# Kernel tuning notes

Hardware: AMD Instinct MI355X
Metric: run time of the kernel (lower is better)

The kernel has to match this reference:

```python
import jax, jax.numpy as jnp
import numpy as np

HIDDEN = 4544
N_HEADS = 71
HEAD_DIM = 64
ROPE_BASE = 10000.0


def _rope_cos_sin(pos, dtype):
    # Falcon rotary embedding for a single decode position `pos`.
    inv_freq = 1.0 / (ROPE_BASE ** (jnp.arange(0, HEAD_DIM, 2, dtype=jnp.float32) / HEAD_DIM))
    freqs = pos * inv_freq                      # [HEAD_DIM/2]
    emb = jnp.concatenate([freqs, freqs])       # [HEAD_DIM]
    return jnp.cos(emb).astype(dtype), jnp.sin(emb).astype(dtype)


def _rotate_half(x):
    x1, x2 = jnp.split(x, 2, axis=-1)
    return jnp.concatenate([-x2, x1], axis=-1)


def setup_inputs() -> dict:
    key = jax.random.key(0)
    ks = jax.random.split(key, 6)
    B = 32
    return {
        "hidden_states": jax.random.normal(ks[0], (1, 1, B, HIDDEN), jnp.float32) * 0.02,
        "attention_mask": jnp.zeros((B, 1, 1, 2048), jnp.float32),
        "w_qkv": jax.random.normal(ks[1], (HIDDEN, (N_HEADS + 2) * HEAD_DIM), jnp.float32) * 0.02,
        "w_dense": jax.random.normal(ks[2], (HIDDEN, HIDDEN), jnp.float32) * 0.02,
        "k_cache": jax.random.normal(ks[3], (B, 1, 2048, HEAD_DIM), jnp.float32),
        "v_cache": jax.random.normal(ks[4], (B, 1, 2048, HEAD_DIM), jnp.float32),
        "layer_past_len": 2047,
    }


def reference(hidden_states, attention_mask, w_qkv, w_dense, k_cache, v_cache, layer_past_len):
    B = hidden_states.shape[2]
    kv_len = layer_past_len + 1
    scalar = 1.0 / np.sqrt(HEAD_DIM)

    x = hidden_states.reshape(B, HIDDEN)                    # decode: [1,1,B,H] -> [B,H]
    qkv = x @ w_qkv                                          # [B, (nh+2)*hd]
    q = qkv[:, : N_HEADS * HEAD_DIM].reshape(B, N_HEADS, HEAD_DIM)
    k = qkv[:, N_HEADS * HEAD_DIM : (N_HEADS + 1) * HEAD_DIM]  # [B, hd] (single MQA KV head)
    v = qkv[:, (N_HEADS + 1) * HEAD_DIM :]                     # [B, hd]

    cos, sin = _rope_cos_sin(jnp.float32(layer_past_len), qkv.dtype)
    q = q * cos + _rotate_half(q) * sin                      # [B, nh, hd]
    k = k * cos + _rotate_half(k) * sin                      # [B, hd]

    # KV-cache scatter update at position layer_past_len
    k_cache = k_cache.at[:, 0, layer_past_len, :].set(k)
    v_cache = v_cache.at[:, 0, layer_past_len, :].set(v)

    keys = k_cache[:, 0, :kv_len, :]                         # [B, L, hd]
    vals = v_cache[:, 0, :kv_len, :]                         # [B, L, hd]

    scores = jnp.einsum("bnh,blh->bnl", q, keys) * scalar    # [B, nh, L]
    scores = scores + attention_mask[:, 0, :, :kv_len]       # mask [B,1,L] broadcast over heads
    probs = jax.nn.softmax(scores, axis=-1)
    ctx = jnp.einsum("bnl,blh->bnh", probs, vals)            # [B, nh, hd]

    out = ctx.reshape(B, HIDDEN) @ w_dense                   # [B, H]
    return out.reshape(1, 1, B, HIDDEN)
```

## Files before the change

### kernel.cpp

```cpp
#include <hip/hip_runtime.h>
#include <math.h>

#define BB    32
#define HID   4544
#define NQKV  4672
#define NKT   71
#define KVCAP 2048

__global__ __launch_bounds__(256) void gemm32v4(
    const float* __restrict__ x, const float* __restrict__ W,
    float* __restrict__ part, int N, int KSG)
{
  __shared__ float xT[64 * 32];
  int lane = threadIdx.x & 63;
  int w    = threadIdx.x >> 6;
  int r0   = w * 8;
  int c0   = blockIdx.x * 256 + lane * 4;
  bool act = c0 < N;
  int cb   = act ? c0 : 0;
  int slice = blockIdx.y;

  float acc[8][4];
#pragma unroll
  for (int r = 0; r < 8; ++r)
#pragma unroll
    for (int j = 0; j < 4; ++j) acc[r][j] = 0.f;

  for (int t = slice; t < NKT; t += KSG) {
    int k0 = t * 64;
    __syncthreads();
    {
      int r  = threadIdx.x & 31;
      int kg = threadIdx.x >> 5;
      const float* xp = x + (size_t)r * HID + k0 + kg * 8;
      float4 a = *(const float4*)xp;
      float4 b = *(const float4*)(xp + 4);
      int kk = kg * 8;
      xT[(kk + 0) * 32 + r] = a.x;
      xT[(kk + 1) * 32 + r] = a.y;
      xT[(kk + 2) * 32 + r] = a.z;
      xT[(kk + 3) * 32 + r] = a.w;
      xT[(kk + 4) * 32 + r] = b.x;
      xT[(kk + 5) * 32 + r] = b.y;
      xT[(kk + 6) * 32 + r] = b.z;
      xT[(kk + 7) * 32 + r] = b.w;
    }
    __syncthreads();

    const float* wp = W + (size_t)k0 * N + cb;

#define FMA_STEP(KK, WV)                                                  \
    {                                                                     \
      float4 xa = *(const float4*)&xT[(KK) * 32 + r0];                    \
      float4 xb = *(const float4*)&xT[(KK) * 32 + r0 + 4];                \
      acc[0][0] = fmaf(xa.x, WV.x, acc[0][0]);                            \
      acc[0][1] = fmaf(xa.x, WV.y, acc[0][1]);                            \
      acc[0][2] = fmaf(xa.x, WV.z, acc[0][2]);                            \
      acc[0][3] = fmaf(xa.x, WV.w, acc[0][3]);                            \
      acc[1][0] = fmaf(xa.y, WV.x, acc[1][0]);                            \
      acc[1][1] = fmaf(xa.y, WV.y, acc[1][1]);                            \
      acc[1][2] = fmaf(xa.y, WV.z, acc[1][2]);                            \
      acc[1][3] = fmaf(xa.y, WV.w, acc[1][3]);                            \
      acc[2][0] = fmaf(xa.z, WV.x, acc[2][0]);                            \
      acc[2][1] = fmaf(xa.z, WV.y, acc[2][1]);                            \
      acc[2][2] = fmaf(xa.z, WV.z, acc[2][2]);                            \
      acc[2][3] = fmaf(xa.z, WV.w, acc[2][3]);                            \
      acc[3][0] = fmaf(xa.w, WV.x, acc[3][0]);                            \
      acc[3][1] = fmaf(xa.w, WV.y, acc[3][1]);                            \
      acc[3][2] = fmaf(xa.w, WV.z, acc[3][2]);                            \
      acc[3][3] = fmaf(xa.w, WV.w, acc[3][3]);                            \
      acc[4][0] = fmaf(xb.x, WV.x, acc[4][0]);                            \
      acc[4][1] = fmaf(xb.x, WV.y, acc[4][1]);                            \
      acc[4][2] = fmaf(xb.x, WV.z, acc[4][2]);                            \
      acc[4][3] = fmaf(xb.x, WV.w, acc[4][3]);                            \
      acc[5][0] = fmaf(xb.y, WV.x, acc[5][0]);                            \
      acc[5][1] = fmaf(xb.y, WV.y, acc[5][1]);                            \
      acc[5][2] = fmaf(xb.y, WV.z, acc[5][2]);                            \
      acc[5][3] = fmaf(xb.y, WV.w, acc[5][3]);                            \
      acc[6][0] = fmaf(xb.z, WV.x, acc[6][0]);                            \
      acc[6][1] = fmaf(xb.z, WV.y, acc[6][1]);                            \
      acc[6][2] = fmaf(xb.z, WV.z, acc[6][2]);                            \
      acc[6][3] = fmaf(xb.z, WV.w, acc[6][3]);                            \
      acc[7][0] = fmaf(xb.w, WV.x, acc[7][0]);                            \
      acc[7][1] = fmaf(xb.w, WV.y, acc[7][1]);                            \
      acc[7][2] = fmaf(xb.w, WV.z, acc[7][2]);                            \
      acc[7][3] = fmaf(xb.w, WV.w, acc[7][3]);                            \
    }

#define LOADW(P, KB)                                                      \
    {                                                                     \
      P##0 = *(const float4*)(wp + (size_t)((KB) + 0) * N);               \
      P##1 = *(const float4*)(wp + (size_t)((KB) + 1) * N);               \
      P##2 = *(const float4*)(wp + (size_t)((KB) + 2) * N);               \
      P##3 = *(const float4*)(wp + (size_t)((KB) + 3) * N);               \
    }
#define FMA4(P, KB)                                                       \
    { FMA_STEP((KB) + 0, P##0) FMA_STEP((KB) + 1, P##1)                   \
      FMA_STEP((KB) + 2, P##2) FMA_STEP((KB) + 3, P##3) }

    float4 A0, A1, A2, A3, B0, B1, B2, B3;
    float4 C0, C1, C2, C3, D0, D1, D2, D3;
    LOADW(A, 0) LOADW(B, 4) LOADW(C, 8) LOADW(D, 12)
    FMA4(A, 0)   LOADW(A, 16)
    FMA4(B, 4)   LOADW(B, 20)
    FMA4(C, 8)   LOADW(C, 24)
    FMA4(D, 12)  LOADW(D, 28)
    FMA4(A, 16)  LOADW(A, 32)
    FMA4(B, 20)  LOADW(B, 36)
    FMA4(C, 24)  LOADW(C, 40)
    FMA4(D, 28)  LOADW(D, 44)
    FMA4(A, 32)  LOADW(A, 48)
    FMA4(B, 36)  LOADW(B, 52)
    FMA4(C, 40)  LOADW(C, 56)
    FMA4(D, 44)  LOADW(D, 60)
    FMA4(A, 48)
    FMA4(B, 52)
    FMA4(C, 56)
    FMA4(D, 60)
#undef FMA_STEP
#undef LOADW
#undef FMA4
  }

  if (act) {
#pragma unroll
    for (int r = 0; r < 8; ++r) {
      float4 v = make_float4(acc[r][0], acc[r][1], acc[r][2], acc[r][3]);
      *(float4*)&part[((size_t)slice * 32 + r0 + r) * N + c0] = v;
    }
  }
}

__global__ __launch_bounds__(256) void qkv_fix(
    const float* __restrict__ part, float* __restrict__ qkvr,
    const int* __restrict__ plen, int KSG)
{
  int u = blockIdx.x * 256 + threadIdx.x;
  int r = u / 2368, t = u % 2368;
  int past = *plen;
  const size_t SS = (size_t)32 * NQKV;

  if (t < 2304) {
    int head = t >> 5, j = t & 31;
    int c0 = head * 64 + j;
    int c1 = c0 + 32;
    const float* p = part + (size_t)r * NQKV;
    float av[8], bv[8];
#pragma unroll
    for (int i = 0; i < 8; ++i) { av[i] = 0.f; bv[i] = 0.f; }
    int s = 0;
    for (; s + 8 <= KSG; s += 8)
#pragma unroll
      for (int i = 0; i < 8; ++i) {
        const float* q = p + (size_t)(s + i) * SS;
        av[i] += q[c0]; bv[i] += q[c1];
      }
    for (; s < KSG; ++s) { av[0] += p[(size_t)s * SS + c0]; bv[0] += p[(size_t)s * SS + c1]; }
    float a = ((av[0]+av[1])+(av[2]+av[3])) + ((av[4]+av[5])+(av[6]+av[7]));
    float b = ((bv[0]+bv[1])+(bv[2]+bv[3])) + ((bv[4]+bv[5])+(bv[6]+bv[7]));
    float invf = (float)pow(10000.0, -(double)j / 32.0);
    float fr   = (float)past * invf;
    float cs = (float)cos((double)fr);
    float sn = (float)sin((double)fr);
    float o0 = a * cs - b * sn;
    float o1 = b * cs + a * sn;
    if (head < 71) { o0 *= 0.125f; o1 *= 0.125f; }
    qkvr[(size_t)r * NQKV + c0] = o0;
    qkvr[(size_t)r * NQKV + c1] = o1;
  } else {
    int c = 4608 + (t - 2304);
    const float* p = part + (size_t)r * NQKV + c;
    float av[8];
#pragma unroll
    for (int i = 0; i < 8; ++i) av[i] = 0.f;
    int s = 0;
    for (; s + 8 <= KSG; s += 8)
#pragma unroll
      for (int i = 0; i < 8; ++i) av[i] += p[(size_t)(s + i) * SS];
    for (; s < KSG; ++s) av[0] += p[(size_t)s * SS];
    qkvr[(size_t)r * NQKV + c] =
        ((av[0]+av[1])+(av[2]+av[3])) + ((av[4]+av[5])+(av[6]+av[7]));
  }
}

__global__ __launch_bounds__(256) void attn_part_k(
    const float* __restrict__ qkvr, const float* __restrict__ kc,
    const float* __restrict__ vc,   const float* __restrict__ mask,
    float* __restrict__ part,       const int* __restrict__ plen)
{
  int b     = blockIdx.x;
  int chunk = blockIdx.y;
  int w     = threadIdx.x >> 6;
  int lane  = threadIdx.x & 63;
  int h0    = w * 18;
  int past  = *plen;
  int kvlen = past + 1;
  int pos0  = chunk * 128;

  __shared__ float qsh[4608];
  __shared__ float pls[4][2][64];

  for (int i = threadIdx.x; i < 1152; i += 256) {
    float4 v = (i < 1136) ? ((const float4*)(qkvr + (size_t)b * NQKV))[i]
                          : make_float4(0.f, 0.f, 0.f, 0.f);
    ((float4*)qsh)[i] = v;
  }
  __syncthreads();

  float lh[18], oh[18];
#pragma unroll
  for (int i = 0; i < 18; ++i) { lh[i] = 0.f; oh[i] = 0.f; }

  for (int sub = 0; sub < 2; ++sub) {
    int sp0 = pos0 + sub * 64;
    if (sp0 >= kvlen) break;
    int pos = sp0 + lane;
    bool valid = pos < kvlen;
    const float* krow = (pos == past)
        ? (qkvr + (size_t)b * NQKV + 4544)
        : (kc + ((size_t)b * KVCAP + pos) * 64);
    float4 ka[16];
#pragma unroll
    for (int j = 0; j < 16; ++j) ka[j] = *(const float4*)(krow + j * 4);

    float vv[64];
#pragma unroll
    for (int p = 0; p < 64; ++p) {
      int pp = sp0 + p;
      const float* vrow = (pp == past)
          ? (qkvr + (size_t)b * NQKV + 4608)
          : (vc + ((size_t)b * KVCAP + pp) * 64);
      vv[p] = vrow[lane];
    }
    float mk = valid ? mask[(size_t)b * KVCAP + pos] : 0.f;

#pragma unroll
    for (int i = 0; i < 18; ++i) {
      int h = h0 + i;
      float s0 = 0.f, s1 = 0.f, s2 = 0.f, s3 = 0.f;
#pragma unroll
      for (int j = 0; j < 16; ++j) {
        float4 qv = *(const float4*)&qsh[h * 64 + j * 4];
        s0 = fmaf(ka[j].x, qv.x, s0);
        s1 = fmaf(ka[j].y, qv.y, s1);
        s2 = fmaf(ka[j].z, qv.z, s2);
        s3 = fmaf(ka[j].w, qv.w, s3);
      }
      float s = (s0 + s1) + (s2 + s3) + mk;
      if (!valid) s = -__builtin_inff();
      float p = __expf(s);

      pls[w][i & 1][lane] = p;
      float o0 = 0.f, o1 = 0.f, o2 = 0.f, o3 = 0.f;
      float la = 0.f, lb = 0.f;
#pragma unroll
      for (int j = 0; j < 16; ++j) {
        float4 pr = *(const float4*)&pls[w][i & 1][j * 4];
        o0 = fmaf(pr.x, vv[j * 4 + 0], o0);
        o1 = fmaf(pr.y, vv[j * 4 + 1], o1);
        o2 = fmaf(pr.z, vv[j * 4 + 2], o2);
        o3 = fmaf(pr.w, vv[j * 4 + 3], o3);
        la += pr.x + pr.y;
        lb += pr.z + pr.w;
      }
      oh[i] += (o0 + o1) + (o2 + o3);
      lh[i] += la + lb;
    }
  }

#pragma unroll
  for (int i = 0; i < 18; ++i) {
    int h = h0 + i;
    if (h >= 71) break;
    size_t base = (((size_t)b * 71 + h) * 16 + chunk) * 65;
    if (lane == 0) part[base] = lh[i];
    part[base + 1 + lane] = oh[i];
  }
}

__global__ __launch_bounds__(256) void attn_comb(
    const float* __restrict__ part, float* __restrict__ ctx)
{
  int u = blockIdx.x * 4 + (threadIdx.x >> 6);
  int lane = threadIdx.x & 63;
  if (u >= BB * 71) return;
  float L0 = 0.f, L1 = 0.f, O0 = 0.f, O1 = 0.f;
#pragma unroll
  for (int c = 0; c < 16; c += 2) {
    size_t b0 = ((size_t)u * 16 + c) * 65;
    size_t b1 = ((size_t)u * 16 + c + 1) * 65;
    L0 += part[b0]; O0 += part[b0 + 1 + lane];
    L1 += part[b1]; O1 += part[b1 + 1 + lane];
  }
  int bb = u / 71, h = u % 71;
  ctx[(size_t)bb * HID + h * 64 + lane] = (O0 + O1) / (L0 + L1);
}

__global__ __launch_bounds__(256) void sum_reduce(
    const float* __restrict__ part, float* __restrict__ out, int KSG)
{
  int u4 = blockIdx.x * 256 + threadIdx.x;
  const size_t SS4 = (size_t)32 * HID / 4;
  const float4* p = (const float4*)part + u4;
  float4 a[8];
#pragma unroll
  for (int i = 0; i < 8; ++i) a[i] = make_float4(0.f, 0.f, 0.f, 0.f);
  int s = 0;
  for (; s + 8 <= KSG; s += 8)
#pragma unroll
    for (int i = 0; i < 8; ++i) {
      float4 v = p[(size_t)(s + i) * SS4];
      a[i].x += v.x; a[i].y += v.y; a[i].z += v.z; a[i].w += v.w;
    }
  for (; s < KSG; ++s) {
    float4 v = p[(size_t)s * SS4];
    a[0].x += v.x; a[0].y += v.y; a[0].z += v.z; a[0].w += v.w;
  }
#pragma unroll
  for (int i = 1; i < 8; ++i) {
    a[0].x += a[i].x; a[0].y += a[i].y; a[0].z += a[i].z; a[0].w += a[i].w;
  }
  ((float4*)out)[u4] = a[0];
}

extern "C" void kernel_launch(void* const* d_in, const int* in_sizes, int n_in,
                              void* d_out, int out_size, void* d_ws, size_t ws_size,
                              hipStream_t stream)
{
  const float* x    = (const float*)d_in[0];
  const float* mask = (const float*)d_in[1];
  const float* wqkv = (const float*)d_in[2];
  const float* wd   = (const float*)d_in[3];
  const float* kc   = (const float*)d_in[4];
  const float* vc   = (const float*)d_in[5];
  const int*   pl   = (const int*)d_in[6];
  float* out = (float*)d_out;
  float* ws  = (float*)d_ws;

  size_t wf = ws_size / 4;
  long avail = (long)wf - 294912;
  long slots = avail / 149504;
  int KSG = (int)(slots < 1 ? 1 : (slots > NKT ? NKT : slots));

  size_t partReg = (size_t)KSG * 149504;
  if (partReg < 4795392) partReg = 4795392;
  float* part = ws;
  float* qkvr = ws + partReg;
  float* ctx  = qkvr + 149504;

  gemm32v4   <<<dim3(19, KSG), 256, 0, stream>>>(x, wqkv, part, NQKV, KSG);
  qkv_fix    <<<296,           256, 0, stream>>>(part, qkvr, pl, KSG);
  attn_part_k<<<dim3(32, 16),  256, 0, stream>>>(qkvr, kc, vc, mask, part, pl);
  attn_comb  <<<568,           256, 0, stream>>>(part, ctx);
  gemm32v4   <<<dim3(18, KSG), 256, 0, stream>>>(ctx, wd, part, HID, KSG);
  sum_reduce <<<142,           256, 0, stream>>>(part, out, KSG);
}
```

Measured before the change: 381.4 us.

## Restructure GEMM tiles to 32 rows per thread, split attention into finer chunks

The GEMM kernel now uses 128-thread blocks where each thread computes all 32 batch rows for 4 columns. Each weight float4 is loaded once per block instead of by every wave, and the loop is a rolling two-row prefetch. Attention doubles the KV chunk count to 32 (64 positions per block) so the grid has more blocks. The combine stage reads 32 partials, and the final reduction uses float2 with twice the blocks. The risks are high register pressure from 128 accumulators and more partial traffic in attention.

```diff
diff --git a/kernel.cpp b/kernel.cpp
--- a/kernel.cpp
+++ b/kernel.cpp
@@ -7,126 +7,84 @@
 #define NKT   71
 #define KVCAP 2048
 
-__global__ __launch_bounds__(256) void gemm32v4(
+__global__ __launch_bounds__(128, 2) void gemm32v5(
     const float* __restrict__ x, const float* __restrict__ W,
     float* __restrict__ part, int N, int KSG)
 {
   __shared__ float xT[64 * 32];
-  int lane = threadIdx.x & 63;
-  int w    = threadIdx.x >> 6;
-  int r0   = w * 8;
-  int c0   = blockIdx.x * 256 + lane * 4;
+  int tid = threadIdx.x;
+  int c0  = blockIdx.x * 512 + tid * 4;
   bool act = c0 < N;
-  int cb   = act ? c0 : 0;
+  int cb  = act ? c0 : 0;
   int slice = blockIdx.y;
 
-  float acc[8][4];
-#pragma unroll
-  for (int r = 0; r < 8; ++r)
+  float acc[32][4];
+#pragma unroll
+  for (int r = 0; r < 32; ++r)
 #pragma unroll
     for (int j = 0; j < 4; ++j) acc[r][j] = 0.f;
+
+  auto ROW = [&](int K, float4 pv) {
+#pragma unroll
+    for (int rg = 0; rg < 8; ++rg) {
+      float4 xv = *(const float4*)&xT[K * 32 + rg * 4];
+#pragma unroll
+      for (int q = 0; q < 4; ++q) {
+        float xs = (q == 0) ? xv.x : (q == 1) ? xv.y : (q == 2) ? xv.z : xv.w;
+        int r = rg * 4 + q;
+        acc[r][0] = fmaf(xs, pv.x, acc[r][0]);
+        acc[r][1] = fmaf(xs, pv.y, acc[r][1]);
+        acc[r][2] = fmaf(xs, pv.z, acc[r][2]);
+        acc[r][3] = fmaf(xs, pv.w, acc[r][3]);
+      }
+    }
+  };
 
   for (int t = slice; t < NKT; t += KSG) {
     int k0 = t * 64;
     __syncthreads();
     {
-      int r  = threadIdx.x & 31;
-      int kg = threadIdx.x >> 5;
-      const float* xp = x + (size_t)r * HID + k0 + kg * 8;
-      float4 a = *(const float4*)xp;
-      float4 b = *(const float4*)(xp + 4);
-      int kk = kg * 8;
-      xT[(kk + 0) * 32 + r] = a.x;
-      xT[(kk + 1) * 32 + r] = a.y;
-      xT[(kk + 2) * 32 + r] = a.z;
-      xT[(kk + 3) * 32 + r] = a.w;
-      xT[(kk + 4) * 32 + r] = b.x;
-      xT[(kk + 5) * 32 + r] = b.y;
-      xT[(kk + 6) * 32 + r] = b.z;
-      xT[(kk + 7) * 32 + r] = b.w;
+      int r  = tid & 31;
+      int kg = tid >> 5;
+      const float* xp = x + (size_t)r * HID + k0 + kg * 16;
+#pragma unroll
+      for (int q = 0; q < 4; ++q) {
+        float4 a = *(const float4*)(xp + q * 4);
+        int kk = kg * 16 + q * 4;
+        xT[(kk + 0) * 32 + r] = a.x;
+        xT[(kk + 1) * 32 + r] = a.y;
+        xT[(kk + 2) * 32 + r] = a.z;
+        xT[(kk + 3) * 32 + r] = a.w;
+      }
     }
     __syncthreads();
 
     const float* wp = W + (size_t)k0 * N + cb;
-
-#define FMA_STEP(KK, WV)                                                  \
-    {                                                                     \
-      float4 xa = *(const float4*)&xT[(KK) * 32 + r0];                    \
-      float4 xb = *(const float4*)&xT[(KK) * 32 + r0 + 4];                \
-      acc[0][0] = fmaf(xa.x, WV.x, acc[0][0]);                            \
-      acc[0][1] = fmaf(xa.x, WV.y, acc[0][1]);                            \
-      acc[0][2] = fmaf(xa.x, WV.z, acc[0][2]);                            \
-      acc[0][3] = fmaf(xa.x, WV.w, acc[0][3]);                            \
-      acc[1][0] = fmaf(xa.y, WV.x, acc[1][0]);                            \
-      acc[1][1] = fmaf(xa.y, WV.y, acc[1][1]);                            \
-      acc[1][2] = fmaf(xa.y, WV.z, acc[1][2]);                            \
-      acc[1][3] = fmaf(xa.y, WV.w, acc[1][3]);                            \
-      acc[2][0] = fmaf(xa.z, WV.x, acc[2][0]);                            \
-      acc[2][1] = fmaf(xa.z, WV.y, acc[2][1]);                            \
-      acc[2][2] = fmaf(xa.z, WV.z, acc[2][2]);                            \
-      acc[2][3] = fmaf(xa.z, WV.w, acc[2][3]);                            \
-      acc[3][0] = fmaf(xa.w, WV.x, acc[3][0]);                            \
-      acc[3][1] = fmaf(xa.w, WV.y, acc[3][1]);                            \
-      acc[3][2] = fmaf(xa.w, WV.z, acc[3][2]);                            \
-      acc[3][3] = fmaf(xa.w, WV.w, acc[3][3]);                            \
-      acc[4][0] = fmaf(xb.x, WV.x, acc[4][0]);                            \
-      acc[4][1] = fmaf(xb.x, WV.y, acc[4][1]);                            \
-      acc[4][2] = fmaf(xb.x, WV.z, acc[4][2]);                            \
-      acc[4][3] = fmaf(xb.x, WV.w, acc[4][3]);                            \
-      acc[5][0] = fmaf(xb.y, WV.x, acc[5][0]);                            \
-      acc[5][1] = fmaf(xb.y, WV.y, acc[5][1]);                            \
-      acc[5][2] = fmaf(xb.y, WV.z, acc[5][2]);                            \
-      acc[5][3] = fmaf(xb.y, WV.w, acc[5][3]);                            \
-      acc[6][0] = fmaf(xb.z, WV.x, acc[6][0]);                            \
-      acc[6][1] = fmaf(xb.z, WV.y, acc[6][1]);                            \
-      acc[6][2] = fmaf(xb.z, WV.z, acc[6][2]);                            \
-      acc[6][3] = fmaf(xb.z, WV.w, acc[6][3]);                            \
-      acc[7][0] = fmaf(xb.w, WV.x, acc[7][0]);                            \
-      acc[7][1] = fmaf(xb.w, WV.y, acc[7][1]);                            \
-      acc[7][2] = fmaf(xb.w, WV.z, acc[7][2]);                            \
-      acc[7][3] = fmaf(xb.w, WV.w, acc[7][3]);                            \
-    }
-
-#define LOADW(P, KB)                                                      \
-    {                                                                     \
-      P##0 = *(const float4*)(wp + (size_t)((KB) + 0) * N);               \
-      P##1 = *(const float4*)(wp + (size_t)((KB) + 1) * N);               \
-      P##2 = *(const float4*)(wp + (size_t)((KB) + 2) * N);               \
-      P##3 = *(const float4*)(wp + (size_t)((KB) + 3) * N);               \
-    }
-#define FMA4(P, KB)                                                       \
-    { FMA_STEP((KB) + 0, P##0) FMA_STEP((KB) + 1, P##1)                   \
-      FMA_STEP((KB) + 2, P##2) FMA_STEP((KB) + 3, P##3) }
-
-    float4 A0, A1, A2, A3, B0, B1, B2, B3;
-    float4 C0, C1, C2, C3, D0, D1, D2, D3;
-    LOADW(A, 0) LOADW(B, 4) LOADW(C, 8) LOADW(D, 12)
-    FMA4(A, 0)   LOADW(A, 16)
-    FMA4(B, 4)   LOADW(B, 20)
-    FMA4(C, 8)   LOADW(C, 24)
-    FMA4(D, 12)  LOADW(D, 28)
-    FMA4(A, 16)  LOADW(A, 32)
-    FMA4(B, 20)  LOADW(B, 36)
-    FMA4(C, 24)  LOADW(C, 40)
-    FMA4(D, 28)  LOADW(D, 44)
-    FMA4(A, 32)  LOADW(A, 48)
-    FMA4(B, 36)  LOADW(B, 52)
-    FMA4(C, 40)  LOADW(C, 56)
-    FMA4(D, 44)  LOADW(D, 60)
-    FMA4(A, 48)
-    FMA4(B, 52)
-    FMA4(C, 56)
-    FMA4(D, 60)
-#undef FMA_STEP
-#undef LOADW
-#undef FMA4
+    float4 p0 = *(const float4*)(wp + 0 * (size_t)N);
+    float4 p1 = *(const float4*)(wp + 1 * (size_t)N);
+    float4 p2 = *(const float4*)(wp + 2 * (size_t)N);
+    float4 p3 = *(const float4*)(wp + 3 * (size_t)N);
+
+#pragma unroll 1
+    for (int k = 0; k < 60; k += 2) {
+      float4 n0 = *(const float4*)(wp + (size_t)(k + 4) * N);
+      float4 n1 = *(const float4*)(wp + (size_t)(k + 5) * N);
+      ROW(k + 0, p0);
+      ROW(k + 1, p1);
+      p0 = p2; p1 = p3; p2 = n0; p3 = n1;
+    }
+    ROW(60, p0);
+    ROW(61, p1);
+    ROW(62, p2);
+    ROW(63, p3);
   }
 
   if (act) {
-#pragma unroll
-    for (int r = 0; r < 8; ++r) {
+    float* pp = part + (size_t)slice * 32 * N + c0;
+#pragma unroll
+    for (int r = 0; r < 32; ++r) {
       float4 v = make_float4(acc[r][0], acc[r][1], acc[r][2], acc[r][3]);
-      *(float4*)&part[((size_t)slice * 32 + r0 + r) * N + c0] = v;
+      *(float4*)(pp + (size_t)r * N) = v;
     }
   }
 }
@@ -195,7 +153,7 @@
   int h0    = w * 18;
   int past  = *plen;
   int kvlen = past + 1;
-  int pos0  = chunk * 128;
+  int pos0  = chunk * 64;
 
   __shared__ float qsh[4608];
   __shared__ float pls[4][2][64];
@@ -207,74 +165,71 @@
   }
   __syncthreads();
 
-  float lh[18], oh[18];
-#pragma unroll
-  for (int i = 0; i < 18; ++i) { lh[i] = 0.f; oh[i] = 0.f; }
-
-  for (int sub = 0; sub < 2; ++sub) {
-    int sp0 = pos0 + sub * 64;
-    if (sp0 >= kvlen) break;
-    int pos = sp0 + lane;
-    bool valid = pos < kvlen;
-    const float* krow = (pos == past)
-        ? (qkvr + (size_t)b * NQKV + 4544)
-        : (kc + ((size_t)b * KVCAP + pos) * 64);
-    float4 ka[16];
-#pragma unroll
-    for (int j = 0; j < 16; ++j) ka[j] = *(const float4*)(krow + j * 4);
-
-    float vv[64];
-#pragma unroll
-    for (int p = 0; p < 64; ++p) {
-      int pp = sp0 + p;
-      const float* vrow = (pp == past)
-          ? (qkvr + (size_t)b * NQKV + 4608)
-          : (vc + ((size_t)b * KVCAP + pp) * 64);
-      vv[p] = vrow[lane];
-    }
-    float mk = valid ? mask[(size_t)b * KVCAP + pos] : 0.f;
-
-#pragma unroll
+  if (pos0 >= kvlen) {
     for (int i = 0; i < 18; ++i) {
       int h = h0 + i;
-      float s0 = 0.f, s1 = 0.f, s2 = 0.f, s3 = 0.f;
-#pragma unroll
-      for (int j = 0; j < 16; ++j) {
-        float4 qv = *(const float4*)&qsh[h * 64 + j * 4];
-        s0 = fmaf(ka[j].x, qv.x, s0);
-        s1 = fmaf(ka[j].y, qv.y, s1);
-        s2 = fmaf(ka[j].z, qv.z, s2);
-        s3 = fmaf(ka[j].w, qv.w, s3);
-      }
-      float s = (s0 + s1) + (s2 + s3) + mk;
-      if (!valid) s = -__builtin_inff();
-      float p = __expf(s);
-
-      pls[w][i & 1][lane] = p;
-      float o0 = 0.f, o1 = 0.f, o2 = 0.f, o3 = 0.f;
-      float la = 0.f, lb = 0.f;
-#pragma unroll
-      for (int j = 0; j < 16; ++j) {
-        float4 pr = *(const float4*)&pls[w][i & 1][j * 4];
-        o0 = fmaf(pr.x, vv[j * 4 + 0], o0);
-        o1 = fmaf(pr.y, vv[j * 4 + 1], o1);
-        o2 = fmaf(pr.z, vv[j * 4 + 2], o2);
-        o3 = fmaf(pr.w, vv[j * 4 + 3], o3);
-        la += pr.x + pr.y;
-        lb += pr.z + pr.w;
-      }
-      oh[i] += (o0 + o1) + (o2 + o3);
-      lh[i] += la + lb;
-    }
-  }
-
-#pragma unroll
+      if (h >= 71) break;
+      size_t base = (((size_t)b * 71 + h) * 32 + chunk) * 65;
+      if (lane == 0) part[base] = 0.f;
+      part[base + 1 + lane] = 0.f;
+    }
+    return;
+  }
+
+  int pos = pos0 + lane;
+  bool valid = pos < kvlen;
+  const float* krow = (pos == past)
+      ? (qkvr + (size_t)b * NQKV + 4544)
+      : (kc + ((size_t)b * KVCAP + pos) * 64);
+  float4 ka[16];
+#pragma unroll
+  for (int j = 0; j < 16; ++j) ka[j] = *(const float4*)(krow + j * 4);
+
+  float vv[64];
+#pragma unroll
+  for (int p = 0; p < 64; ++p) {
+    int pp = pos0 + p;
+    const float* vrow = (pp == past)
+        ? (qkvr + (size_t)b * NQKV + 4608)
+        : (vc + ((size_t)b * KVCAP + pp) * 64);
+    vv[p] = vrow[lane];
+  }
+  float mk = valid ? mask[(size_t)b * KVCAP + pos] : 0.f;
+
+#pragma unroll 2
   for (int i = 0; i < 18; ++i) {
     int h = h0 + i;
-    if (h >= 71) break;
-    size_t base = (((size_t)b * 71 + h) * 16 + chunk) * 65;
-    if (lane == 0) part[base] = lh[i];
-    part[base + 1 + lane] = oh[i];
+    float s0 = 0.f, s1 = 0.f, s2 = 0.f, s3 = 0.f;
+#pragma unroll
+    for (int j = 0; j < 16; ++j) {
+      float4 qv = *(const float4*)&qsh[h * 64 + j * 4];
+      s0 = fmaf(ka[j].x, qv.x, s0);
+      s1 = fmaf(ka[j].y, qv.y, s1);
+      s2 = fmaf(ka[j].z, qv.z, s2);
+      s3 = fmaf(ka[j].w, qv.w, s3);
+    }
+    float s = (s0 + s1) + (s2 + s3) + mk;
+    if (!valid) s = -__builtin_inff();
+    float p = __expf(s);
+
+    pls[w][i & 1][lane] = p;
+    float o0 = 0.f, o1 = 0.f, o2 = 0.f, o3 = 0.f;
+    float la = 0.f, lb = 0.f;
+#pragma unroll
+    for (int j = 0; j < 16; ++j) {
+      float4 pr = *(const float4*)&pls[w][i & 1][j * 4];
+      o0 = fmaf(pr.x, vv[j * 4 + 0], o0);
+      o1 = fmaf(pr.y, vv[j * 4 + 1], o1);
+      o2 = fmaf(pr.z, vv[j * 4 + 2], o2);
+      o3 = fmaf(pr.w, vv[j * 4 + 3], o3);
+      la += pr.x + pr.y;
+      lb += pr.z + pr.w;
+    }
+    if (h < 71) {
+      size_t base = (((size_t)b * 71 + h) * 32 + chunk) * 65;
+      if (lane == 0) part[base] = la + lb;
+      part[base + 1 + lane] = (o0 + o1) + (o2 + o3);
+    }
   }
 }
 
@@ -286,9 +241,9 @@
   if (u >= BB * 71) return;
   float L0 = 0.f, L1 = 0.f, O0 = 0.f, O1 = 0.f;
 #pragma unroll
-  for (int c = 0; c < 16; c += 2) {
-    size_t b0 = ((size_t)u * 16 + c) * 65;
-    size_t b1 = ((size_t)u * 16 + c + 1) * 65;
+  for (int c = 0; c < 32; c += 2) {
+    size_t b0 = ((size_t)u * 32 + c) * 65;
+    size_t b1 = ((size_t)u * 32 + c + 1) * 65;
     L0 += part[b0]; O0 += part[b0 + 1 + lane];
     L1 += part[b1]; O1 += part[b1 + 1 + lane];
   }
@@ -299,28 +254,26 @@
 __global__ __launch_bounds__(256) void sum_reduce(
     const float* __restrict__ part, float* __restrict__ out, int KSG)
 {
-  int u4 = blockIdx.x * 256 + threadIdx.x;
-  const size_t SS4 = (size_t)32 * HID / 4;
-  const float4* p = (const float4*)part + u4;
-  float4 a[8];
-#pragma unroll
-  for (int i = 0; i < 8; ++i) a[i] = make_float4(0.f, 0.f, 0.f, 0.f);
+  int u2 = blockIdx.x * 256 + threadIdx.x;
+  const size_t SS2 = (size_t)32 * HID / 2;
+  const float2* p = (const float2*)part + u2;
+  float2 a[8];
+#pragma unroll
+  for (int i = 0; i < 8; ++i) a[i] = make_float2(0.f, 0.f);
   int s = 0;
   for (; s + 8 <= KSG; s += 8)
 #pragma unroll
     for (int i = 0; i < 8; ++i) {
-      float4 v = p[(size_t)(s + i) * SS4];
-      a[i].x += v.x; a[i].y += v.y; a[i].z += v.z; a[i].w += v.w;
+      float2 v = p[(size_t)(s + i) * SS2];
+      a[i].x += v.x; a[i].y += v.y;
     }
   for (; s < KSG; ++s) {
-    float4 v = p[(size_t)s * SS4];
-    a[0].x += v.x; a[0].y += v.y; a[0].z += v.z; a[0].w += v.w;
-  }
-#pragma unroll
-  for (int i = 1; i < 8; ++i) {
-    a[0].x += a[i].x; a[0].y += a[i].y; a[0].z += a[i].z; a[0].w += a[i].w;
-  }
-  ((float4*)out)[u4] = a[0];
+    float2 v = p[(size_t)s * SS2];
+    a[0].x += v.x; a[0].y += v.y;
+  }
+#pragma unroll
+  for (int i = 1; i < 8; ++i) { a[0].x += a[i].x; a[0].y += a[i].y; }
+  ((float2*)out)[u2] = a[0];
 }
 
 extern "C" void kernel_launch(void* const* d_in, const int* in_sizes, int n_in,
@@ -348,10 +301,10 @@
   float* qkvr = ws + partReg;
   float* ctx  = qkvr + 149504;
 
-  gemm32v4   <<<dim3(19, KSG), 256, 0, stream>>>(x, wqkv, part, NQKV, KSG);
+  gemm32v5   <<<dim3(10, KSG), 128, 0, stream>>>(x, wqkv, part, NQKV, KSG);
   qkv_fix    <<<296,           256, 0, stream>>>(part, qkvr, pl, KSG);
-  attn_part_k<<<dim3(32, 16),  256, 0, stream>>>(qkvr, kc, vc, mask, part, pl);
+  attn_part_k<<<dim3(32, 32),  256, 0, stream>>>(qkvr, kc, vc, mask, part, pl);
   attn_comb  <<<568,           256, 0, stream>>>(part, ctx);
-  gemm32v4   <<<dim3(18, KSG), 256, 0, stream>>>(ctx, wd, part, HID, KSG);
-  sum_reduce <<<142,           256, 0, stream>>>(part, out, KSG);
-}
+  gemm32v5   <<<dim3(9, KSG),  128, 0, stream>>>(ctx, wd, part, HID, KSG);
+  sum_reduce <<<284,           256, 0, stream>>>(part, out, KSG);
+}
```

New measurement: 328.9 us. -13.7%, faster.
